# Optimization experiments

Measured on AMD Instinct MI355X. Metric: run time of the kernel, lower is better.

The kernel has to match this reference:

```python
import jax, jax.numpy as jnp
import numpy as np

B, S, D_IN, D_E, H = 512, 100, 300, 150, 2  # batch, patches, patch feat, embed half, heads
L = S + 1  # 101 tokens with class token
EPS = 1e-5


def setup_inputs() -> dict:
    key = jax.random.key(0)
    ks = jax.random.split(key, 12)
    r = lambda k, shp, s=0.02: (jax.random.normal(k, shp, jnp.float32) * s)
    return {
        "x": jax.random.normal(ks[0], (B, S, D_IN), jnp.float32),
        "Wp": r(ks[1], (D_IN, D_E)), "bp": jnp.zeros((D_E,), jnp.float32),
        "pos_table": r(ks[2], (L, D_E), 1.0),
        "class_embed": r(ks[3], (D_E,), 1.0),
        "Wq": r(ks[4], (H, 2 * D_E, 2 * D_E)),
        "Wk": r(ks[5], (H, 2 * D_E, 2 * D_E)),
        "Wv": r(ks[6], (H, 2 * D_E, 2 * D_E)),
        "bn1_g": jnp.ones((L,), jnp.float32), "bn1_b": jnp.zeros((L,), jnp.float32),
        "Wp1": r(ks[7], (900, 300)), "bp1": jnp.zeros((300,), jnp.float32),
        "bn2_g": jnp.ones((L,), jnp.float32), "bn2_b": jnp.zeros((L,), jnp.float32),
        "fc1_W": r(ks[8], (1200, 512)), "fc1_b": jnp.zeros((512,), jnp.float32),
        "fc2_W": r(ks[9], (512, 2)), "fc2_b": jnp.zeros((2,), jnp.float32),
    }


def _batchnorm(x, g, b):
    # torch BatchNorm1d(101) on [B, 101, F]: normalize per channel (dim 1) over (B, F), training-mode batch stats
    mean = jnp.mean(x, axis=(0, 2), keepdims=True)
    var = jnp.var(x, axis=(0, 2), keepdims=True)
    return (x - mean) * jax.lax.rsqrt(var + EPS) * g[None, :, None] + b[None, :, None]


def reference(x, Wp, bp, pos_table, class_embed, Wq, Wk, Wv, bn1_g, bn1_b,
              Wp1, bp1, bn2_g, bn2_b, fc1_W, fc1_b, fc2_W, fc2_b):
    h = jax.nn.relu(x @ Wp + bp)                                   # [B,100,150]
    cls = jnp.concatenate([jnp.broadcast_to(class_embed, (B, D_E)),
                           jnp.broadcast_to(pos_table[0], (B, D_E))], axis=-1)   # [B,300]
    tok = jnp.concatenate([h, jnp.broadcast_to(pos_table[1:], (B, S, D_E))], axis=-1)  # [B,100,300]
    z = jnp.concatenate([cls[:, None, :], tok], axis=1)            # [B,101,300]
    skip1 = jax.lax.stop_gradient(z)                               # x.clone().detach()

    # multi-head self-attention (per-head Q/K/V, no 1/sqrt(d) scaling, matching source)
    Q = jnp.einsum('bsd,hde->hbse', z, Wq)                         # [H,B,101,300]
    K = jnp.einsum('bsd,hde->hbse', z, Wk)
    V = jnp.einsum('bsd,hde->hbse', z, Wv)
    attn = jax.nn.softmax(jnp.einsum('hbse,hbte->hbst', Q, K), axis=-1)  # [H,B,101,101]
    o = jnp.einsum('hbst,hbte->hbse', attn, V)                     # [H,B,101,300]
    msa = jnp.transpose(o, (1, 2, 0, 3)).reshape(B, L, H * 2 * D_E)  # concat heads -> [B,101,600]

    y = _batchnorm(msa, bn1_g, bn1_b)
    y = jnp.concatenate([y, skip1], axis=-1)                       # [B,101,900]
    skip2 = jax.lax.stop_gradient(y)
    y = jax.nn.relu(y @ Wp1 + bp1)                                 # [B,101,300]
    y = _batchnorm(y, bn2_g, bn2_b)
    y = jnp.concatenate([y, skip2], axis=-1)                       # [B,101,1200]
    out = (y[:, 0, :] @ fc1_W + fc1_b) @ fc2_W + fc2_b             # [B,2]
    return out
```

## Files before the change

kernel.cpp:

```cpp
#include <hip/hip_runtime.h>
#include <hip/hip_fp16.h>
#include <math.h>

#define BB 512
#define SS 100
#define DE 150
#define DM 300
#define LL 101
#define NH 2

typedef _Float16 f16x8 __attribute__((ext_vector_type(8)));
typedef float f32x4 __attribute__((ext_vector_type(4)));

#define WS_CLS    0
#define WS_QK     320
#define WS_S0     960
#define WS_CPOS   964
#define WS_CVEC   1200
#define WS_COLSUM 1536
#define WS_CST0   1856
#define WS_STATS  1860
#define WS_G      2176
#define WS_Q0     4608
#define WS_P3     5248
#define WS_PART1  14336
#define WS_PART2  15360
#define WS_MSA    16384
#define WS_Y1     (WS_MSA + 512*600)
#define WS_WPF    477184

__global__ void kC1(const float* __restrict__ pos, const float* __restrict__ cle,
                    const float* __restrict__ Wq, const float* __restrict__ Wp1,
                    const float* __restrict__ Wp,
                    const float* __restrict__ f1W, const float* __restrict__ f2W,
                    const float* __restrict__ f1b, const float* __restrict__ f2b,
                    float* __restrict__ ws) {
  __shared__ float cls[DM];
  int b = blockIdx.x, tid = threadIdx.x;
  if (b < 18) {
    for (int i = tid; i < DM; i += 256) cls[i] = (i < DE) ? cle[i] : pos[i - DE];
    __syncthreads();
  }
  if (b < 3) {
    int idx = b * 256 + tid;
    if (idx < NH * DM) {
      int h = idx / DM, e = idx % DM;
      const float* w = Wq + h * DM * DM + e;
      float acc = 0.f;
      for (int d = 0; d < DM; ++d) acc += cls[d] * w[d * DM];
      ws[WS_Q0 + idx] = acc;
    }
  } else if (b < 18) {
    int kb = b - 3;
    for (int n = tid; n < DM; n += 256) {
      float cs = 0.f, cv = 0.f;
      for (int k = kb * 60; k < kb * 60 + 60; ++k) {
        float w = Wp1[k * 300 + n];
        if (k < 600) cs += w; else cv += cls[k - 600] * w;
      }
      ws[WS_P3 + kb * 600 + n] = cs;
      ws[WS_P3 + kb * 600 + 300 + n] = cv;
    }
  } else if (b == 18) {
    for (int i = tid; i < DM; i += 256)
      ws[WS_CLS + i] = (i < DE) ? cle[i] : pos[i - DE];
  } else if (b < 29) {
    int t = (b - 19) * 256 + tid;
    if (t < 2400) {
      int k = t >> 1, c = t & 1;
      const float* r = f1W + k * 512;
      float acc = 0.f;
      for (int m = 0; m < 512; ++m) acc += r[m] * f2W[m * 2 + c];
      ws[WS_G + t] = acc;
    } else if (t < 2402) {
      int c = t - 2400;
      float acc = f2b[c];
      for (int m = 0; m < 512; ++m) acc += f1b[m] * f2W[m * 2 + c];
      ws[WS_CST0 + c] = acc;
    }
  } else {
    int idx = (b - 29) * 256 + tid;
    int kq = idx / 160, n = idx % 160;
    f16x8 pk;
#pragma unroll
    for (int j = 0; j < 8; ++j) {
      int k = kq * 8 + j;
      float v = (k < DM && n < DE) ? Wp[k * DE + n] : 0.f;
      pk[j] = (_Float16)v;
    }
    *(f16x8*)((char*)ws + (size_t)WS_WPF * 4 + (size_t)idx * 16) = pk;
  }
}

__global__ void kC2(const float* __restrict__ Wk, float* __restrict__ ws) {
  __shared__ float q0s[NH * DM];
  int tid = threadIdx.x;
  for (int i = tid; i < NH * DM; i += 256) q0s[i] = ws[WS_Q0 + i];
  __syncthreads();
  int wave = tid >> 6, lane = tid & 63;
  int idx = blockIdx.x * 4 + wave;
  int h = idx / DM, d = idx % DM;
  const float* w = Wk + h * DM * DM + d * DM;
  const float* q = q0s + h * DM;
  float acc = 0.f;
  for (int e = lane; e < DM; e += 64) acc += w[e] * q[e];
  for (int o = 32; o; o >>= 1) acc += __shfl_xor(acc, o);
  if (!lane) ws[WS_QK + idx] = acc;
}

__global__ void kC3(const float* __restrict__ pos, const float* __restrict__ bp1,
                    float* __restrict__ ws) {
  int b = blockIdx.x, tid = threadIdx.x;
  int wave = tid >> 6, lane = tid & 63;
  if (b < 50) {
    int idx = b * 4 + wave;
    int tt = idx >> 1, h = idx & 1;
    const float* pr = pos + (tt + 1) * DE;
    const float* qk = ws + WS_QK + h * DM + DE;
    float acc = 0.f;
    for (int j = lane; j < DE; j += 64) acc += pr[j] * qk[j];
    for (int o = 32; o; o >>= 1) acc += __shfl_xor(acc, o);
    if (!lane) ws[WS_CPOS + idx] = acc;
  } else if (b == 50) {
    if (wave < NH) {
      float acc = 0.f;
      for (int d = lane; d < DM; d += 64) acc += ws[WS_CLS + d] * ws[WS_QK + wave * DM + d];
      for (int o = 32; o; o >>= 1) acc += __shfl_xor(acc, o);
      if (!lane) ws[WS_S0 + wave] = acc;
    }
  } else {
    for (int n = tid; n < DM; n += 256) {
      float cs = 0.f, cv = bp1[n];
      for (int p = 0; p < 15; ++p) {
        cs += ws[WS_P3 + p * 600 + n];
        cv += ws[WS_P3 + p * 600 + 300 + n];
      }
      ws[WS_COLSUM + n] = cs;
      ws[WS_CVEC + n] = cv;
    }
  }
}

__launch_bounds__(512, 4)
__global__ void kA(const float* __restrict__ x, const float* __restrict__ bp,
                   const float* __restrict__ pos, const float* __restrict__ Wv,
                   float* __restrict__ ws) {
  __shared__ __align__(16) char smem[44000];
  __half (*hb)[DE + 2] = (__half(*)[DE + 2])smem;
  _Float16* wpt0 = (_Float16*)(smem);
  _Float16* xs0  = (_Float16*)(smem + 10240);
  _Float16* wpt1 = (_Float16*)(smem + 18240);
  _Float16* xs1  = (_Float16*)(smem + 28480);
  float* aux = (float*)(smem + 36480);
  float* zb  = (float*)(smem + 41600);

  int b = blockIdx.x, tid = threadIdx.x;
  int w = tid >> 6, lane = tid & 63;
  int l16 = lane & 15, lg = lane >> 4;
  int wm = w >> 2, wn = w & 3;
  int nnt = (wn < 3) ? 3 : 1;
  int nt0 = (wn < 3) ? wn * 3 : 9;

  const float* xb = x + b * (SS * DM);
  const char* wpf = (const char*)ws + (size_t)WS_WPF * 4;
  int rowl[4];
#pragma unroll
  for (int mt = 0; mt < 4; ++mt) {
    int r = wm * 64 + mt * 16 + l16;
    rowl[mt] = (r < SS) ? r : (SS - 1);
  }

  f32x4 acc[4][3];
#pragma unroll
  for (int mt = 0; mt < 4; ++mt)
#pragma unroll
    for (int nti = 0; nti < 3; ++nti) acc[mt][nti] = (f32x4){0.f, 0.f, 0.f, 0.f};

  float xr[4][2];
  float4 wa, wb2;

#define XLOAD(S)                                                               \
  { int kc_ = (S) * 32;                                                        \
    _Pragma("unroll")                                                          \
    for (int i_ = 0; i_ < 4; ++i_) {                                           \
      int t_ = tid + 512 * i_;                                                 \
      if (t_ < 1600) {                                                         \
        int r_ = t_ >> 4, c_ = t_ & 15, k_ = kc_ + 2 * c_;                     \
        if (k_ + 1 < DM) {                                                     \
          float2 v_ = *(const float2*)(xb + r_ * DM + k_);                     \
          xr[i_][0] = v_.x; xr[i_][1] = v_.y;                                  \
        } else {                                                               \
          xr[i_][0] = (k_ < DM) ? xb[r_ * DM + k_] : 0.f;                      \
          xr[i_][1] = 0.f;                                                     \
        } } } }

#define XWRITE(XP)                                                             \
  { _Pragma("unroll")                                                          \
    for (int i_ = 0; i_ < 4; ++i_) {                                           \
      int t_ = tid + 512 * i_;                                                 \
      if (t_ < 1600) {                                                         \
        int r_ = t_ >> 4, c_ = t_ & 15;                                        \
        *(__half2*)((char*)(XP) + r_ * 80 + c_ * 4) =                          \
            __floats2half2_rn(xr[i_][0], xr[i_][1]);                           \
      } } }

#define WLOAD(S)                                                               \
  { const char* s_ = wpf + (size_t)(S) * 10240;                                \
    wa = *(const float4*)(s_ + tid * 16);                                      \
    if (tid < 128) wb2 = *(const float4*)(s_ + (tid + 512) * 16); }

#define WWRITE(WP)                                                             \
  { *(float4*)((char*)(WP) + tid * 16) = wa;                                   \
    if (tid < 128) *(float4*)((char*)(WP) + (tid + 512) * 16) = wb2; }

  XLOAD(0); WLOAD(0);
  XWRITE(xs0); WWRITE(wpt0);
  __syncthreads();

  for (int s = 0; s < 10; ++s) {
    _Float16* wc = (s & 1) ? wpt1 : wpt0;
    _Float16* xc = (s & 1) ? xs1 : xs0;
    _Float16* wnx = (s & 1) ? wpt0 : wpt1;
    _Float16* xnx = (s & 1) ? xs0 : xs1;
    if (s < 9) { WLOAD(s + 1); XLOAD(s + 1); }
    f16x8 Bf[3];
#pragma unroll
    for (int nti = 0; nti < 3; ++nti)
      if (nti < nnt)
        Bf[nti] = *(const f16x8*)(wc + ((lg * 160 + (nt0 + nti) * 16 + l16) * 8));
#pragma unroll
    for (int mt = 0; mt < 4; ++mt) {
      f16x8 Af = *(const f16x8*)(xc + rowl[mt] * 40 + lg * 8);
#pragma unroll
      for (int nti = 0; nti < 3; ++nti)
        if (nti < nnt)
          acc[mt][nti] = __builtin_amdgcn_mfma_f32_16x16x32_f16(Af, Bf[nti], acc[mt][nti], 0, 0, 0);
    }
    if (s < 9) { WWRITE(wnx); XWRITE(xnx); }
    __syncthreads();
  }

#pragma unroll
  for (int nti = 0; nti < 3; ++nti) {
    if (nti < nnt) {
      int col = (nt0 + nti) * 16 + l16;
      float bpv = (col < DE) ? bp[col] : 0.f;
#pragma unroll
      for (int mt = 0; mt < 4; ++mt) {
        int rbase = wm * 64 + mt * 16 + lg * 4;
        f32x4 v = acc[mt][nti];
#pragma unroll
        for (int reg = 0; reg < 4; ++reg) {
          int row = rbase + reg;
          if (row < SS && col < DE) {
            float hv = v[reg] + bpv;
            hb[row][col] = __float2half(hv > 0.f ? hv : 0.f);
          }
        }
      }
    }
  }
  for (int i = tid; i < DM; i += 512) {
    aux[i] = ws[WS_QK + (i / DE) * DM + (i % DE)];
    aux[DM + i] = ws[WS_CLS + i];
  }
  __syncthreads();

  if (tid < NH * SS) {
    int hh = tid / SS, tt = tid % SS;
    const __half2* hr = (const __half2*)&hb[tt][0];
    const float* qr = &aux[hh * DE];
    float s = 0.f;
    for (int j2 = 0; j2 < DE / 2; ++j2) {
      float2 hv = __half22float2(hr[j2]);
      float2 qv = *(const float2*)&qr[2 * j2];
      s += hv.x * qv.x + hv.y * qv.y;
    }
    aux[600 + hh * LL + tt + 1] = s + ws[WS_CPOS + tt * NH + hh];
  } else if (tid < NH * SS + NH) {
    int hh = tid - NH * SS;
    aux[600 + hh * LL] = ws[WS_S0 + hh];
  }
  __syncthreads();

  if (w < NH) {
    float v0 = aux[600 + w * LL + lane];
    float v1 = (lane + 64 < LL) ? aux[600 + w * LL + lane + 64] : -1e30f;
    float m = fmaxf(v0, v1);
    for (int o = 32; o; o >>= 1) m = fmaxf(m, __shfl_xor(m, o));
    float e0 = expf(v0 - m);
    float e1 = (lane + 64 < LL) ? expf(v1 - m) : 0.f;
    float s = e0 + e1;
    for (int o = 32; o; o >>= 1) s += __shfl_xor(s, o);
    float inv = 1.f / s;
    aux[802 + w * LL + lane] = e0 * inv;
    if (lane + 64 < LL) aux[802 + w * LL + lane + 64] = e1 * inv;
  }
  __syncthreads();

  for (int o = tid; o < NH * DM; o += 512) {
    int hh = o / DM, d = o % DM;
    const float* p = &aux[802 + hh * LL];
    float acc2 = p[0] * aux[DM + d];
    if (d < DE) {
      for (int t = 1; t <= SS; ++t) acc2 += p[t] * __half2float(hb[t - 1][d]);
    } else {
      int dd = d - DE;
      for (int t = 1; t <= SS; ++t) acc2 += p[t] * pos[t * DE + dd];
    }
    zb[o] = acc2;
  }
  __syncthreads();

  float s_ = 0.f, ss_ = 0.f;
  for (int e = tid; e < NH * DM; e += 512) {
    int hh = e / DM, ee = e % DM;
    const float* wv = Wv + hh * DM * DM + ee;
    const float* z = zb + hh * DM;
    float t0 = 0.f, t1 = 0.f;
    for (int d = 0; d < DM; d += 2) {
      t0 += z[d] * wv[d * DM];
      t1 += z[d + 1] * wv[(d + 1) * DM];
    }
    float val = t0 + t1;
    ws[WS_MSA + b * 600 + e] = val;
    s_ += val; ss_ += val * val;
  }
  for (int o = 32; o; o >>= 1) { s_ += __shfl_xor(s_, o); ss_ += __shfl_xor(ss_, o); }
  if (!lane) { aux[1100 + w] = s_; aux[1108 + w] = ss_; }
  __syncthreads();
  if (!tid) {
    float S = 0.f, SS2 = 0.f;
    for (int i = 0; i < 8; ++i) { S += aux[1100 + i]; SS2 += aux[1108 + i]; }
    ws[WS_PART1 + b * 2] = S;
    ws[WS_PART1 + b * 2 + 1] = SS2;
  }
}

__launch_bounds__(512)
__global__ void k5(const float* __restrict__ Wp1, const float* __restrict__ g1,
                   const float* __restrict__ b1, float* __restrict__ ws) {
  __shared__ float ab[2][600];
  __shared__ float part[2][2][300];
  __shared__ float sh[2][8];
  __shared__ float s_a1, s_b1;
  int b0 = blockIdx.x * 2, tid = threadIdx.x;
  int wv = tid >> 6, ln = tid & 63;
  for (int i = tid; i < 1200; i += 512) ab[i / 600][i % 600] = ws[WS_MSA + b0 * 600 + i];
  {
    float s = ws[WS_PART1 + tid * 2], ss = ws[WS_PART1 + tid * 2 + 1];
    for (int o = 32; o; o >>= 1) { s += __shfl_xor(s, o); ss += __shfl_xor(ss, o); }
    if (!ln) { sh[0][wv] = s; sh[1][wv] = ss; }
  }
  __syncthreads();
  if (!tid) {
    float S = 0.f, SS2 = 0.f;
    for (int i = 0; i < 8; ++i) { S += sh[0][i]; SS2 += sh[1][i]; }
    float n = (float)(BB * 600);
    float mean = S / n, var = SS2 / n - mean * mean;
    float a = (1.f / sqrtf(var + 1e-5f)) * g1[0];
    s_a1 = a; s_b1 = b1[0] - a * mean;
    if (blockIdx.x == 0) { ws[WS_STATS + 0] = a; ws[WS_STATS + 1] = s_b1; }
  }
  __syncthreads();
  int g = tid >> 8, t = tid & 255;
  int kbeg = g * 300, kend = kbeg + 300;
  for (int n = t; n < 300; n += 256) {
    float a0 = 0.f, a1v = 0.f;
    for (int k = kbeg; k < kend; ++k) {
      float wq = Wp1[k * 300 + n];
      a0 += ab[0][k] * wq;
      a1v += ab[1][k] * wq;
    }
    part[g][0][n] = a0;
    part[g][1][n] = a1v;
  }
  __syncthreads();
  float a1 = s_a1, beta1 = s_b1;
  float s2 = 0.f, ss2 = 0.f;
  for (int n = tid; n < 300; n += 512) {
    float c = beta1 * ws[WS_COLSUM + n] + ws[WS_CVEC + n];
    float v0 = a1 * (part[0][0][n] + part[1][0][n]) + c;
    float v1 = a1 * (part[0][1][n] + part[1][1][n]) + c;
    v0 = v0 > 0.f ? v0 : 0.f;
    v1 = v1 > 0.f ? v1 : 0.f;
    ws[WS_Y1 + b0 * 300 + n] = v0;
    ws[WS_Y1 + (b0 + 1) * 300 + n] = v1;
    s2 += v0 + v1; ss2 += v0 * v0 + v1 * v1;
  }
  for (int o = 32; o; o >>= 1) { s2 += __shfl_xor(s2, o); ss2 += __shfl_xor(ss2, o); }
  if (!ln) { sh[0][wv] = s2; sh[1][wv] = ss2; }
  __syncthreads();
  if (!tid) {
    float S = 0.f, SS2 = 0.f;
    for (int i = 0; i < 8; ++i) { S += sh[0][i]; SS2 += sh[1][i]; }
    ws[WS_PART2 + blockIdx.x * 2] = S;
    ws[WS_PART2 + blockIdx.x * 2 + 1] = SS2;
  }
}

__launch_bounds__(256)
__global__ void k7(const float* __restrict__ g2, const float* __restrict__ b2,
                   float* __restrict__ out, const float* __restrict__ ws) {
  __shared__ float Gs[2400];
  __shared__ float sh[2][4];
  __shared__ float cc[4];
  int tid = threadIdx.x, wv = tid >> 6, ln = tid & 63;
  for (int i = tid; i < 2400; i += 256) Gs[i] = ws[WS_G + i];
  {
    float s = ws[WS_PART2 + tid * 2], ss = ws[WS_PART2 + tid * 2 + 1];
    for (int o = 32; o; o >>= 1) { s += __shfl_xor(s, o); ss += __shfl_xor(ss, o); }
    if (!ln) { sh[0][wv] = s; sh[1][wv] = ss; }
  }
  __syncthreads();
  if (!tid) {
    float S = 0.f, SS2 = 0.f;
    for (int i = 0; i < 4; ++i) { S += sh[0][i]; SS2 += sh[1][i]; }
    float n = (float)(BB * 300);
    float mean = S / n, var = SS2 / n - mean * mean;
    float a = (1.f / sqrtf(var + 1e-5f)) * g2[0];
    cc[0] = a; cc[1] = b2[0] - a * mean;
  }
  __syncthreads();
  if (tid < 2) {
    int c = tid;
    float sg1 = 0.f, sg2 = 0.f, sg3 = 0.f;
    for (int k = 0; k < 300; ++k) sg1 += Gs[k * 2 + c];
    for (int k = 300; k < 900; ++k) sg2 += Gs[k * 2 + c];
    for (int j = 0; j < 300; ++j) sg3 += ws[WS_CLS + j] * Gs[(900 + j) * 2 + c];
    cc[2 + c] = ws[WS_CST0 + c] + sg3 + cc[1] * sg1 + ws[WS_STATS + 1] * sg2;
  }
  __syncthreads();
  int b = blockIdx.x * 4 + wv;
  float a1 = ws[WS_STATS + 0], a2 = cc[0];
  const float* y1 = ws + WS_Y1 + b * 300;
  const float* ms = ws + WS_MSA + b * 600;
  float o0 = 0.f, o1 = 0.f, p0 = 0.f, p1 = 0.f;
  for (int k = ln; k < 300; k += 64) { float v = y1[k]; o0 += v * Gs[k * 2]; o1 += v * Gs[k * 2 + 1]; }
  for (int j = ln; j < 600; j += 64) { float v = ms[j]; p0 += v * Gs[(300 + j) * 2]; p1 += v * Gs[(300 + j) * 2 + 1]; }
  for (int o = 32; o; o >>= 1) {
    o0 += __shfl_xor(o0, o); o1 += __shfl_xor(o1, o);
    p0 += __shfl_xor(p0, o); p1 += __shfl_xor(p1, o);
  }
  if (!ln) {
    out[b * 2] = a2 * o0 + a1 * p0 + cc[2];
    out[b * 2 + 1] = a2 * o1 + a1 * p1 + cc[3];
  }
}

extern "C" void kernel_launch(void* const* d_in, const int* in_sizes, int n_in,
                              void* d_out, int out_size, void* d_ws, size_t ws_size,
                              hipStream_t stream) {
  const float* x    = (const float*)d_in[0];
  const float* Wp   = (const float*)d_in[1];
  const float* bp   = (const float*)d_in[2];
  const float* pos  = (const float*)d_in[3];
  const float* cle  = (const float*)d_in[4];
  const float* Wq   = (const float*)d_in[5];
  const float* Wk   = (const float*)d_in[6];
  const float* Wv   = (const float*)d_in[7];
  const float* bn1g = (const float*)d_in[8];
  const float* bn1b = (const float*)d_in[9];
  const float* Wp1  = (const float*)d_in[10];
  const float* bp1  = (const float*)d_in[11];
  const float* bn2g = (const float*)d_in[12];
  const float* bn2b = (const float*)d_in[13];
  const float* f1W  = (const float*)d_in[14];
  const float* f1b  = (const float*)d_in[15];
  const float* f2W  = (const float*)d_in[16];
  const float* f2b  = (const float*)d_in[17];
  float* ws = (float*)d_ws;
  float* out = (float*)d_out;

  hipLaunchKernelGGL(kC1, dim3(54), dim3(256), 0, stream, pos, cle, Wq, Wp1, Wp, f1W, f2W, f1b, f2b, ws);
  hipLaunchKernelGGL(kC2, dim3(150), dim3(256), 0, stream, Wk, ws);
  hipLaunchKernelGGL(kC3, dim3(52), dim3(256), 0, stream, pos, bp1, ws);
  hipLaunchKernelGGL(kA, dim3(512), dim3(512), 0, stream, x, bp, pos, Wv, ws);
  hipLaunchKernelGGL(k5, dim3(256), dim3(512), 0, stream, Wp1, bn1g, bn1b, ws);
  hipLaunchKernelGGL(k7, dim3(128), dim3(256), 0, stream, bn2g, bn2b, out, ws);
}
```

Baseline: 119.5 us.

## Batch the class-token V projection into a separate fp16 MFMA GEMM kernel

The per-sample scalar matvec of the attention output with Wv, which had every block of kA stream Wv from global memory, is moved into a new kernel kV. That kernel runs a batched fp16 MFMA GEMM over all 512 samples using an fp16 Wv copy packed in the prep kernel. kA now writes its attention-weighted vectors as fp16 to the workspace, and the BN1 partial sums are reduced over 16 blocks instead of 512. The cost is an extra launch, a global round trip for the intermediate, and fp16 precision in the V projection.

```diff
diff --git a/kernel.cpp b/kernel.cpp
--- a/kernel.cpp
+++ b/kernel.cpp
@@ -28,10 +28,12 @@
 #define WS_MSA    16384
 #define WS_Y1     (WS_MSA + 512*600)
 #define WS_WPF    477184
+#define WS_WVF    502784
+#define WS_ZB16   605184
 
 __global__ void kC1(const float* __restrict__ pos, const float* __restrict__ cle,
                     const float* __restrict__ Wq, const float* __restrict__ Wp1,
-                    const float* __restrict__ Wp,
+                    const float* __restrict__ Wp, const float* __restrict__ Wv,
                     const float* __restrict__ f1W, const float* __restrict__ f2W,
                     const float* __restrict__ f1b, const float* __restrict__ f2b,
                     float* __restrict__ ws) {
@@ -78,7 +80,7 @@
       for (int m = 0; m < 512; ++m) acc += f1b[m] * f2W[m * 2 + c];
       ws[WS_CST0 + c] = acc;
     }
-  } else {
+  } else if (b < 54) {
     int idx = (b - 29) * 256 + tid;
     int kq = idx / 160, n = idx % 160;
     f16x8 pk;
@@ -89,6 +91,18 @@
       pk[j] = (_Float16)v;
     }
     *(f16x8*)((char*)ws + (size_t)WS_WPF * 4 + (size_t)idx * 16) = pk;
+  } else {
+    int idx = (b - 54) * 256 + tid;
+    int h = idx / 12800, rem = idx % 12800;
+    int kq = rem / 320, n = rem % 320;
+    f16x8 pk;
+#pragma unroll
+    for (int j = 0; j < 8; ++j) {
+      int k = kq * 8 + j;
+      float v = (k < DM && n < DM) ? Wv[h * DM * DM + k * DM + n] : 0.f;
+      pk[j] = (_Float16)v;
+    }
+    *(f16x8*)((char*)ws + (size_t)WS_WVF * 4 + (size_t)idx * 16) = pk;
   }
 }
 
@@ -143,16 +157,14 @@
 
 __launch_bounds__(512, 4)
 __global__ void kA(const float* __restrict__ x, const float* __restrict__ bp,
-                   const float* __restrict__ pos, const float* __restrict__ Wv,
-                   float* __restrict__ ws) {
-  __shared__ __align__(16) char smem[44000];
+                   const float* __restrict__ pos, float* __restrict__ ws) {
+  __shared__ __align__(16) char smem[41600];
   __half (*hb)[DE + 2] = (__half(*)[DE + 2])smem;
   _Float16* wpt0 = (_Float16*)(smem);
   _Float16* xs0  = (_Float16*)(smem + 10240);
   _Float16* wpt1 = (_Float16*)(smem + 18240);
   _Float16* xs1  = (_Float16*)(smem + 28480);
   float* aux = (float*)(smem + 36480);
-  float* zb  = (float*)(smem + 41600);
 
   int b = blockIdx.x, tid = threadIdx.x;
   int w = tid >> 6, lane = tid & 63;
@@ -298,6 +310,7 @@
   }
   __syncthreads();
 
+  __half* zb16 = (__half*)((char*)ws + (size_t)WS_ZB16 * 4);
   for (int o = tid; o < NH * DM; o += 512) {
     int hh = o / DM, d = o % DM;
     const float* p = &aux[802 + hh * LL];
@@ -308,32 +321,87 @@
       int dd = d - DE;
       for (int t = 1; t <= SS; ++t) acc2 += p[t] * pos[t * DE + dd];
     }
-    zb[o] = acc2;
-  }
-  __syncthreads();
+    zb16[((size_t)hh * 512 + b) * 320 + d] = __float2half(acc2);
+  }
+  if (tid < 40) {
+    int hh = tid / 20, dd = 300 + tid % 20;
+    zb16[((size_t)hh * 512 + b) * 320 + dd] = __float2half(0.f);
+  }
+}
+
+__launch_bounds__(512, 4)
+__global__ void kV(float* __restrict__ ws) {
+  __shared__ float shp[2][8];
+  int blk = blockIdx.x;
+  int mtile = blk >> 2, nb = (blk >> 1) & 1, h = blk & 1;
+  int tid = threadIdx.x;
+  int w = tid >> 6, lane = tid & 63;
+  int l16 = lane & 15, lg = lane >> 4;
+  int wm = w >> 2, wn = w & 3;
+  int nnt = (wn < 3) ? 3 : 1;
+  int nt0 = (wn < 3) ? wn * 3 : 9;
+  int mbase = mtile * 128;
+
+  const __half* zb16 = (const __half*)((const char*)ws + (size_t)WS_ZB16 * 4) + (size_t)h * 512 * 320;
+  const __half* wvf  = (const __half*)((const char*)ws + (size_t)WS_WVF * 4) + (size_t)h * 40 * 320 * 8;
+
+  int brow[4];
+#pragma unroll
+  for (int mt = 0; mt < 4; ++mt) brow[mt] = mbase + wm * 64 + mt * 16 + l16;
+
+  f32x4 acc[4][3];
+#pragma unroll
+  for (int mt = 0; mt < 4; ++mt)
+#pragma unroll
+    for (int nti = 0; nti < 3; ++nti) acc[mt][nti] = (f32x4){0.f, 0.f, 0.f, 0.f};
+
+  for (int s = 0; s < 10; ++s) {
+    f16x8 Bf[3];
+#pragma unroll
+    for (int nti = 0; nti < 3; ++nti)
+      if (nti < nnt) {
+        int n = nb * 160 + (nt0 + nti) * 16 + l16;
+        Bf[nti] = *(const f16x8*)&wvf[((size_t)(s * 4 + lg) * 320 + n) * 8];
+      }
+#pragma unroll
+    for (int mt = 0; mt < 4; ++mt) {
+      f16x8 Af = *(const f16x8*)&zb16[(size_t)brow[mt] * 320 + s * 32 + lg * 8];
+#pragma unroll
+      for (int nti = 0; nti < 3; ++nti)
+        if (nti < nnt)
+          acc[mt][nti] = __builtin_amdgcn_mfma_f32_16x16x32_f16(Af, Bf[nti], acc[mt][nti], 0, 0, 0);
+    }
+  }
 
   float s_ = 0.f, ss_ = 0.f;
-  for (int e = tid; e < NH * DM; e += 512) {
-    int hh = e / DM, ee = e % DM;
-    const float* wv = Wv + hh * DM * DM + ee;
-    const float* z = zb + hh * DM;
-    float t0 = 0.f, t1 = 0.f;
-    for (int d = 0; d < DM; d += 2) {
-      t0 += z[d] * wv[d * DM];
-      t1 += z[d + 1] * wv[(d + 1) * DM];
-    }
-    float val = t0 + t1;
-    ws[WS_MSA + b * 600 + e] = val;
-    s_ += val; ss_ += val * val;
+#pragma unroll
+  for (int nti = 0; nti < 3; ++nti) {
+    if (nti < nnt) {
+      int col = nb * 160 + (nt0 + nti) * 16 + l16;
+      if (col < DM) {
+#pragma unroll
+        for (int mt = 0; mt < 4; ++mt) {
+          int rbase = mbase + wm * 64 + mt * 16 + lg * 4;
+          f32x4 v = acc[mt][nti];
+#pragma unroll
+          for (int reg = 0; reg < 4; ++reg) {
+            int row = rbase + reg;
+            float val = v[reg];
+            ws[WS_MSA + row * 600 + h * DM + col] = val;
+            s_ += val; ss_ += val * val;
+          }
+        }
+      }
+    }
   }
   for (int o = 32; o; o >>= 1) { s_ += __shfl_xor(s_, o); ss_ += __shfl_xor(ss_, o); }
-  if (!lane) { aux[1100 + w] = s_; aux[1108 + w] = ss_; }
+  if (!lane) { shp[0][w] = s_; shp[1][w] = ss_; }
   __syncthreads();
   if (!tid) {
     float S = 0.f, SS2 = 0.f;
-    for (int i = 0; i < 8; ++i) { S += aux[1100 + i]; SS2 += aux[1108 + i]; }
-    ws[WS_PART1 + b * 2] = S;
-    ws[WS_PART1 + b * 2 + 1] = SS2;
+    for (int i = 0; i < 8; ++i) { S += shp[0][i]; SS2 += shp[1][i]; }
+    ws[WS_PART1 + blk * 2] = S;
+    ws[WS_PART1 + blk * 2 + 1] = SS2;
   }
 }
 
@@ -348,7 +416,8 @@
   int wv = tid >> 6, ln = tid & 63;
   for (int i = tid; i < 1200; i += 512) ab[i / 600][i % 600] = ws[WS_MSA + b0 * 600 + i];
   {
-    float s = ws[WS_PART1 + tid * 2], ss = ws[WS_PART1 + tid * 2 + 1];
+    float s = 0.f, ss = 0.f;
+    if (tid < 16) { s = ws[WS_PART1 + tid * 2]; ss = ws[WS_PART1 + tid * 2 + 1]; }
     for (int o = 32; o; o >>= 1) { s += __shfl_xor(s, o); ss += __shfl_xor(ss, o); }
     if (!ln) { sh[0][wv] = s; sh[1][wv] = ss; }
   }
@@ -472,10 +541,11 @@
   float* ws = (float*)d_ws;
   float* out = (float*)d_out;
 
-  hipLaunchKernelGGL(kC1, dim3(54), dim3(256), 0, stream, pos, cle, Wq, Wp1, Wp, f1W, f2W, f1b, f2b, ws);
+  hipLaunchKernelGGL(kC1, dim3(154), dim3(256), 0, stream, pos, cle, Wq, Wp1, Wp, Wv, f1W, f2W, f1b, f2b, ws);
   hipLaunchKernelGGL(kC2, dim3(150), dim3(256), 0, stream, Wk, ws);
   hipLaunchKernelGGL(kC3, dim3(52), dim3(256), 0, stream, pos, bp1, ws);
-  hipLaunchKernelGGL(kA, dim3(512), dim3(512), 0, stream, x, bp, pos, Wv, ws);
+  hipLaunchKernelGGL(kA, dim3(512), dim3(512), 0, stream, x, bp, pos, ws);
+  hipLaunchKernelGGL(kV, dim3(16), dim3(512), 0, stream, ws);
   hipLaunchKernelGGL(k5, dim3(256), dim3(512), 0, stream, Wp1, bn1g, bn1b, ws);
   hipLaunchKernelGGL(k7, dim3(128), dim3(256), 0, stream, bn2g, bn2b, out, ws);
 }
```

After: 117.3 us. No clear change (-1.9%).
